# Performance work log

Measured on AMD Instinct MI355X. Metric: run time of the kernel, lower is better.

The kernel has to match this reference:

```python
import jax, jax.numpy as jnp
import numpy as np

GAMMA = 1.4
CFL = 0.5
DX = 1e-3
ENTROPY_FIX = 0.1
NX = 1048576


def _roe_flux(rL, uL, pL, rR, uR, pR):
    """Roe flux with Harten entropy fix, vectorized over all interfaces."""
    g = GAMMA
    EL = pL / (g - 1) + 0.5 * rL * uL * uL
    ER = pR / (g - 1) + 0.5 * rR * uR * uR
    HL = (EL + pL) / rL
    HR = (ER + pR) / rR
    sL = jnp.sqrt(rL)
    sR = jnp.sqrt(rR)
    den = sL + sR
    ur = (sL * uL + sR * uR) / den
    Hr = (sL * HL + sR * HR) / den
    c = jnp.sqrt(jnp.clip((g - 1) * (Hr - 0.5 * ur * ur), 1e-10))
    eps = ENTROPY_FIX * c
    l1 = ur - c
    l3 = ur + c
    a1 = jnp.sqrt(l1 * l1 + eps * eps)
    a2 = jnp.sqrt(ur * ur + eps * eps)
    a3 = jnp.sqrt(l3 * l3 + eps * eps)
    drho = rR - rL
    du = uR - uL
    dp = pR - pL
    c2 = c * c
    al2 = drho - dp / c2
    al1 = (dp - c * rR * du) / (2 * c2)
    al3 = (dp + c * rR * du) / (2 * c2)
    FrL = rL * uL; FmL = rL * uL * uL + pL; FeL = uL * (EL + pL)
    FrR = rR * uR; FmR = rR * uR * uR + pR; FeR = uR * (ER + pR)
    dr = a1 * al1 + a2 * al2 + a3 * al3
    dm = a1 * al1 * l1 + a2 * al2 * ur + a3 * al3 * l3
    de = (a1 * al1 * (Hr - ur * c) + a2 * al2 * 0.5 * ur * ur
          + a3 * al3 * (Hr + ur * c))
    return (0.5 * (FrL + FrR - dr),
            0.5 * (FmL + FmR - dm),
            0.5 * (FeL + FeR - de))


def _step(carry, t_final):
    """One first-order Euler timestep with CFL-adaptive dt clipped to t_final."""
    rho, rhou, E, t = carry
    g = GAMMA
    u = rhou / rho
    p = (g - 1) * (E - 0.5 * rho * u * u)
    c = jnp.sqrt(g * p / rho)
    dt = CFL * DX / jnp.max(jnp.abs(u) + c)
    dt = jnp.minimum(dt, jnp.maximum(t_final - t, 0.0))
    # replicate edge ghost cells: [nx] -> [nx+2]
    rp = jnp.concatenate([rho[:1], rho, rho[-1:]])
    up = jnp.concatenate([u[:1], u, u[-1:]])
    pp = jnp.concatenate([p[:1], p, p[-1:]])
    # nx+1 interface fluxes
    Fr, Fm, Fe = _roe_flux(rp[:-1], up[:-1], pp[:-1], rp[1:], up[1:], pp[1:])
    dtdx = dt / DX
    return (rho - dtdx * (Fr[1:] - Fr[:-1]),
            rhou - dtdx * (Fm[1:] - Fm[:-1]),
            E - dtdx * (Fe[1:] - Fe[:-1]),
            t + dt)


def setup_inputs() -> dict:
    key = jax.random.key(0)
    k1, k2, k3 = jax.random.split(key, 3)
    rho = 1.0 + 0.5 * jax.random.uniform(k1, (NX,), jnp.float32)
    u = 0.1 * jax.random.normal(k2, (NX,), jnp.float32)
    p = 1.0 + 0.5 * jax.random.uniform(k3, (NX,), jnp.float32)
    return {"rho_init": rho, "u_init": u, "p_init": p,
            "t_final": jnp.float32(10.0), "n_steps": 32}


def reference(rho_init, u_init, p_init, t_final, n_steps):
    g = GAMMA
    rho = rho_init
    rhou = rho_init * u_init
    E = p_init / (g - 1) + 0.5 * rho_init * u_init ** 2
    body = jax.checkpoint(lambda c, _: (_step(c, t_final), None))
    (rho, rhou, E, _), _ = jax.lax.scan(
        body, (rho, rhou, E, jnp.float32(0.0)), None, length=n_steps)
    u = rhou / rho
    p = (g - 1) * (E - 0.5 * rho * u * u)
    return rho, u, p
```

## Files before the change

kernel.cpp:

```cpp
#include <hip/hip_runtime.h>


#define NXC   1048576
#define GAM   1.4f
#define GM1   0.4f
#define IGM1  2.5f
#define CFLC  0.5f
#define DXC   1e-3f
#define IDXC  1000.0f
#define EFIX  0.1f
#define NSTEPS 32
#define NSLOT  (NSTEPS + 1)

#define ABLK  1024
#define ACPT  4
#define ATILE (ABLK*ACPT)
#define ANBLK (NXC/ATILE)

#define CTRL_TOTAL (NSLOT * ANBLK)

__device__ __forceinline__ float frcp(float x){ return __builtin_amdgcn_rcpf(x); }
__device__ __forceinline__ float frsq(float x){ return __builtin_amdgcn_rsqf(x); }
__device__ __forceinline__ float fsqrt_(float x){ return __builtin_amdgcn_sqrtf(x); }

__device__ __forceinline__ float devloadf(const float* p) {
    return __hip_atomic_load(p, __ATOMIC_RELAXED, __HIP_MEMORY_SCOPE_AGENT);
}
__device__ __forceinline__ void devstoref(float* p, float v) {
    __hip_atomic_store(p, v, __ATOMIC_RELAXED, __HIP_MEMORY_SCOPE_AGENT);
}
__device__ __forceinline__ unsigned devloadu(const unsigned* p) {
    return __hip_atomic_load(p, __ATOMIC_RELAXED, __HIP_MEMORY_SCOPE_AGENT);
}
__device__ __forceinline__ void devstoreu(unsigned* p, unsigned v) {
    __hip_atomic_store(p, v, __ATOMIC_RELAXED, __HIP_MEMORY_SCOPE_AGENT);
}

__device__ __forceinline__ float wave_max(float v) {
    #pragma unroll
    for (int k = 32; k >= 1; k >>= 1)
        v = fmaxf(v, __shfl_xor(v, k));
    return v;
}

__global__ void bmax_init(unsigned* z) {
    int i = blockIdx.x * 256 + threadIdx.x;
    if (i < CTRL_TOTAL) z[i] = 0xAAAAAAAAu;
}

__device__ __forceinline__ void roe(
        float rL, float uL, float pL, float sL, float gL,
        float rR, float uR, float pR, float sR, float gR,
        float& Frj, float& Fmj, float& Fej) {
    float invden = frcp(sL + sR);
    float ur = (sL * uL + sR * uR) * invden;
    float Hr = (gL + gR) * invden;
    float c2u = fmaxf(GM1 * (Hr - 0.5f * ur * ur), 1e-10f);
    float qc = frsq(c2u);
    float c  = c2u * qc;
    float inv2c2 = 0.5f * qc * qc;
    float eps = EFIX * c;
    float l1 = ur - c, l3 = ur + c;
    float a1 = fsqrt_(l1 * l1 + eps * eps);
    float a2 = fsqrt_(ur * ur + eps * eps);
    float a3 = fsqrt_(l3 * l3 + eps * eps);
    float drho = rR - rL;
    float du   = uR - uL;
    float dp   = pR - pL;
    float al2 = drho - (dp + dp) * inv2c2;
    float tcd = c * rR * du;
    float al1 = (dp - tcd) * inv2c2;
    float al3 = (dp + tcd) * inv2c2;
    float FrL = rL * uL, FrR = rR * uR;
    float FmL = FrL * uL + pL, FmR = FrR * uR + pR;
    float FeL = uL * (gL * sL), FeR = uR * (gR * sR);
    float w1 = a1 * al1, w2 = a2 * al2, w3 = a3 * al3;
    Frj = 0.5f * (FrL + FrR - (w1 + w2 + w3));
    Fmj = 0.5f * (FmL + FmR - (w1 * l1 + w2 * ur + w3 * l3));
    Fej = 0.5f * (FeL + FeR - (w1 * (Hr - ur * c) + w2 * (0.5f * ur * ur)
                               + w3 * (Hr + ur * c)));
}

__global__ __launch_bounds__(ABLK, 4) void euler_async(
        const float* __restrict__ rho0, const float* __restrict__ u0,
        const float* __restrict__ p0, const float* __restrict__ tf,
        float* __restrict__ out, unsigned* __restrict__ bmax,
        float* __restrict__ halo) {
    __shared__ float Lr[ABLK], Lu[ABLK], Lp[ABLK];
    __shared__ float fxr[ABLK], fxm[ABLK], fxe[ABLK];
    __shared__ float red[ABLK / 64];
    __shared__ float samax;

    const int tid = threadIdx.x;
    const int lb = (blockIdx.x & 7) * (ANBLK / 8) + (blockIdx.x >> 3);
    const int c0 = lb * ATILE + ACPT * tid;
    const int lane = tid & 63, wid = tid >> 6;

    float cr[4], cu[4], cp[4], cE[4], cs[4], cg[4];

    {
        float4 r4 = *(const float4*)(rho0 + c0);
        float4 u4 = *(const float4*)(u0 + c0);
        float4 p4 = *(const float4*)(p0 + c0);
        cr[0]=r4.x; cr[1]=r4.y; cr[2]=r4.z; cr[3]=r4.w;
        cu[0]=u4.x; cu[1]=u4.y; cu[2]=u4.z; cu[3]=u4.w;
        cp[0]=p4.x; cp[1]=p4.y; cp[2]=p4.z; cp[3]=p4.w;
        float nm = 0.f;
        #pragma unroll
        for (int c = 0; c < 4; ++c) {
            float E = cp[c] * IGM1 + 0.5f * cr[c] * cu[c] * cu[c];
            float q = frsq(cr[c]);
            cE[c] = E;
            cs[c] = cr[c] * q;
            cg[c] = (E + cp[c]) * q;
            nm = fmaxf(nm, fabsf(cu[c]) + fsqrt_(GAM * cp[c] * (q * q)));
        }
        Lr[tid]=cr[3]; Lu[tid]=cu[3]; Lp[tid]=cp[3];
        if (tid == 0) {
            float* h = halo + (size_t)lb * 6;
            devstoref(h, cr[0]); devstoref(h+1, cu[0]); devstoref(h+2, cp[0]);
        }
        if (tid == ABLK - 1) {
            float* h = halo + (size_t)lb * 6 + 3;
            devstoref(h, cr[3]); devstoref(h+1, cu[3]); devstoref(h+2, cp[3]);
        }
        nm = wave_max(nm);
        if (lane == 0) red[wid] = nm;
        __syncthreads();
        if (tid < ABLK / 64) {
            float bm = red[tid];
            bm = fmaxf(bm, __shfl_xor(bm, 8));
            bm = fmaxf(bm, __shfl_xor(bm, 4));
            bm = fmaxf(bm, __shfl_xor(bm, 2));
            bm = fmaxf(bm, __shfl_xor(bm, 1));
            if (tid == 0) devstoreu(&bmax[lb], __float_as_uint(bm));
        }
    }
    float t = 0.f;
    const float tfin = *tf;

    for (int k = 0; k < NSTEPS; ++k) {
        const unsigned* brow = bmax + (size_t)k * ANBLK;
        const unsigned* brdt = bmax + (size_t)(k > 0 ? k - 1 : 0) * ANBLK;
        float Fr[5], Fm[5], Fe[5];

        float rl, ul, pl;
        float r5 = 0.f, u5 = 0.f, p5 = 0.f;
        if (tid == 0) {
            if (lb > 0) {
                while (devloadu(&brow[lb - 1]) & 0x80000000u)
                    __builtin_amdgcn_s_sleep(1);
                const float* h = halo + ((size_t)k * ANBLK + (lb - 1)) * 6 + 3;
                rl = devloadf(h); ul = devloadf(h+1); pl = devloadf(h+2);
            } else { rl = cr[0]; ul = cu[0]; pl = cp[0]; }
        } else { rl = Lr[tid-1]; ul = Lu[tid-1]; pl = Lp[tid-1]; }
        if (tid == ABLK - 1) {
            if (lb < ANBLK - 1) {
                while (devloadu(&brow[lb + 1]) & 0x80000000u)
                    __builtin_amdgcn_s_sleep(1);
                const float* h = halo + ((size_t)k * ANBLK + (lb + 1)) * 6;
                r5 = devloadf(h); u5 = devloadf(h+1); p5 = devloadf(h+2);
            } else { r5 = cr[3]; u5 = cu[3]; p5 = cp[3]; }
        }

        roe(cr[0],cu[0],cp[0],cs[0],cg[0], cr[1],cu[1],cp[1],cs[1],cg[1],
            Fr[1], Fm[1], Fe[1]);
        roe(cr[1],cu[1],cp[1],cs[1],cg[1], cr[2],cu[2],cp[2],cs[2],cg[2],
            Fr[2], Fm[2], Fe[2]);
        roe(cr[2],cu[2],cp[2],cs[2],cg[2], cr[3],cu[3],cp[3],cs[3],cg[3],
            Fr[3], Fm[3], Fe[3]);

        {
            float El = pl * IGM1 + 0.5f * rl * ul * ul;
            float ql = frsq(rl);
            float sl = rl * ql, gl = (El + pl) * ql;
            roe(rl,ul,pl,sl,gl, cr[0],cu[0],cp[0],cs[0],cg[0],
                Fr[0], Fm[0], Fe[0]);
            fxr[tid] = Fr[0]; fxm[tid] = Fm[0]; fxe[tid] = Fe[0];
        }

        if (tid == ABLK - 1) {
            float E5 = p5 * IGM1 + 0.5f * r5 * u5 * u5;
            float q5 = frsq(r5);
            float s5 = r5 * q5, g5 = (E5 + p5) * q5;
            roe(cr[3],cu[3],cp[3],cs[3],cg[3], r5,u5,p5,s5,g5,
                Fr[4], Fm[4], Fe[4]);
        }

        if (wid == 0) {
            unsigned v0, v1, v2, v3;
            for (;;) {
                v0 = devloadu(&brdt[lane]);
                v1 = devloadu(&brdt[64 + lane]);
                v2 = devloadu(&brdt[128 + lane]);
                v3 = devloadu(&brdt[192 + lane]);
                if (__all(((v0 | v1 | v2 | v3) & 0x80000000u) == 0u)) break;
                __builtin_amdgcn_s_sleep(1);
            }
            float m = fmaxf(fmaxf(__uint_as_float(v0), __uint_as_float(v1)),
                            fmaxf(__uint_as_float(v2), __uint_as_float(v3)));
            m = wave_max(m);
            if (lane == 0) samax = m;
        }

        __syncthreads();

        if (tid < ABLK - 1) {
            Fr[4] = fxr[tid + 1]; Fm[4] = fxm[tid + 1]; Fe[4] = fxe[tid + 1];
        }
        float amax = samax;
        float dt = fminf((CFLC * DXC) * frcp(amax), fmaxf(tfin - t, 0.f));
        t += dt;
        float dtdx = dt * IDXC;

        float nm = 0.f;
        #pragma unroll
        for (int c = 0; c < 4; ++c) {
            float r2 = cr[c]         - dtdx * (Fr[c+1] - Fr[c]);
            float m2 = cr[c] * cu[c] - dtdx * (Fm[c+1] - Fm[c]);
            float E2 = cE[c]         - dtdx * (Fe[c+1] - Fe[c]);
            float q2 = frsq(r2);
            float ir = q2 * q2;
            float u2 = m2 * ir;
            float p2 = GM1 * (E2 - 0.5f * r2 * u2 * u2);
            cr[c]=r2; cu[c]=u2; cp[c]=p2; cE[c]=E2;
            cs[c]=r2 * q2;
            cg[c]=(E2 + p2) * q2;
            nm = fmaxf(nm, fabsf(u2) + fsqrt_(GAM * p2 * ir));
        }

        if (k < NSTEPS - 1) {
            Lr[tid]=cr[3]; Lu[tid]=cu[3]; Lp[tid]=cp[3];
            if (tid == 0) {
                float* h = halo + ((size_t)(k + 1) * ANBLK + lb) * 6;
                devstoref(h, cr[0]); devstoref(h+1, cu[0]); devstoref(h+2, cp[0]);
            }
            if (tid == ABLK - 1) {
                float* h = halo + ((size_t)(k + 1) * ANBLK + lb) * 6 + 3;
                devstoref(h, cr[3]); devstoref(h+1, cu[3]); devstoref(h+2, cp[3]);
            }
            nm = wave_max(nm);
            if (lane == 0) red[wid] = nm;
            __syncthreads();
            if (tid < ABLK / 64) {
                float bm = red[tid];
                bm = fmaxf(bm, __shfl_xor(bm, 8));
                bm = fmaxf(bm, __shfl_xor(bm, 4));
                bm = fmaxf(bm, __shfl_xor(bm, 2));
                bm = fmaxf(bm, __shfl_xor(bm, 1));
                if (tid == 0)
                    devstoreu(&bmax[(size_t)(k + 1) * ANBLK + lb],
                              __float_as_uint(bm));
            }
        } else {
            *(float4*)(out + c0)         = make_float4(cr[0], cr[1], cr[2], cr[3]);
            *(float4*)(out + NXC + c0)   = make_float4(cu[0], cu[1], cu[2], cu[3]);
            *(float4*)(out + 2*NXC + c0) = make_float4(cp[0], cp[1], cp[2], cp[3]);
        }
    }
}

extern "C" void kernel_launch(void* const* d_in, const int* in_sizes, int n_in,
                              void* d_out, int out_size, void* d_ws, size_t ws_size,
                              hipStream_t stream) {
    const float* rho0 = (const float*)d_in[0];
    const float* u0   = (const float*)d_in[1];
    const float* p0   = (const float*)d_in[2];
    const float* tf   = (const float*)d_in[3];

    float* out      = (float*)d_out;
    unsigned* bmax  = (unsigned*)d_ws;
    float* halo     = (float*)(bmax + CTRL_TOTAL);

    bmax_init<<<(CTRL_TOTAL + 255) / 256, 256, 0, stream>>>(bmax);

    void* args[] = {(void*)&rho0, (void*)&u0, (void*)&p0, (void*)&tf,
                    (void*)&out, (void*)&bmax, (void*)&halo};
    hipLaunchCooperativeKernel((void*)euler_async, dim3(ANBLK), dim3(ABLK),
                               args, 0, stream);
}
```

Before: 203.1 us.

## Exchange neighbor states via wave shuffles and drop one block barrier per step

Replaces the per-thread shared-memory exchange of left-neighbor states and interface fluxes with intra-wave shuffles, passing only wave-boundary values through small double-buffered shared arrays. This removes one __syncthreads per timestep, and every wave now polls the global block-max array itself, with loads issued early so they overlap the Roe flux work. The block-reduction result is written by wave 8 instead of wave 0, moving that work off wave 0, which holds the halo thread. The costs are more global polling traffic, since all 16 waves per block read 256 entries, and reliance on double buffering for correctness.

```diff
diff --git a/kernel.cpp b/kernel.cpp
--- a/kernel.cpp
+++ b/kernel.cpp
@@ -16,6 +16,7 @@
 #define ACPT  4
 #define ATILE (ABLK*ACPT)
 #define ANBLK (NXC/ATILE)
+#define NWAVE (ABLK/64)
 
 #define CTRL_TOTAL (NSLOT * ANBLK)
 
@@ -86,10 +87,9 @@
         const float* __restrict__ p0, const float* __restrict__ tf,
         float* __restrict__ out, unsigned* __restrict__ bmax,
         float* __restrict__ halo) {
-    __shared__ float Lr[ABLK], Lu[ABLK], Lp[ABLK];
-    __shared__ float fxr[ABLK], fxm[ABLK], fxe[ABLK];
-    __shared__ float red[ABLK / 64];
-    __shared__ float samax;
+    __shared__ float W3[2][NWAVE][5];
+    __shared__ float R0[2][NWAVE][5];
+    __shared__ float red[2][NWAVE];
 
     const int tid = threadIdx.x;
     const int lb = (blockIdx.x & 7) * (ANBLK / 8) + (blockIdx.x >> 3);
@@ -115,7 +115,14 @@
             cg[c] = (E + cp[c]) * q;
             nm = fmaxf(nm, fabsf(cu[c]) + fsqrt_(GAM * cp[c] * (q * q)));
         }
-        Lr[tid]=cr[3]; Lu[tid]=cu[3]; Lp[tid]=cp[3];
+        if (lane == 63) {
+            W3[0][wid][0]=cr[3]; W3[0][wid][1]=cu[3]; W3[0][wid][2]=cp[3];
+            W3[0][wid][3]=cs[3]; W3[0][wid][4]=cg[3];
+        }
+        if (lane == 0) {
+            R0[0][wid][0]=cr[0]; R0[0][wid][1]=cu[0]; R0[0][wid][2]=cp[0];
+            R0[0][wid][3]=cs[0]; R0[0][wid][4]=cg[0];
+        }
         if (tid == 0) {
             float* h = halo + (size_t)lb * 6;
             devstoref(h, cr[0]); devstoref(h+1, cu[0]); devstoref(h+2, cp[0]);
@@ -125,15 +132,15 @@
             devstoref(h, cr[3]); devstoref(h+1, cu[3]); devstoref(h+2, cp[3]);
         }
         nm = wave_max(nm);
-        if (lane == 0) red[wid] = nm;
+        if (lane == 0) red[0][wid] = nm;
         __syncthreads();
-        if (tid < ABLK / 64) {
-            float bm = red[tid];
+        if (wid == 8 && lane < NWAVE) {
+            float bm = red[0][lane];
             bm = fmaxf(bm, __shfl_xor(bm, 8));
             bm = fmaxf(bm, __shfl_xor(bm, 4));
             bm = fmaxf(bm, __shfl_xor(bm, 2));
             bm = fmaxf(bm, __shfl_xor(bm, 1));
-            if (tid == 0) devstoreu(&bmax[lb], __float_as_uint(bm));
+            if (lane == 0) devstoreu(&bmax[lb], __float_as_uint(bm));
         }
     }
     float t = 0.f;
@@ -142,26 +149,59 @@
     for (int k = 0; k < NSTEPS; ++k) {
         const unsigned* brow = bmax + (size_t)k * ANBLK;
         const unsigned* brdt = bmax + (size_t)(k > 0 ? k - 1 : 0) * ANBLK;
+        const int kb = k & 1;
         float Fr[5], Fm[5], Fe[5];
 
-        float rl, ul, pl;
-        float r5 = 0.f, u5 = 0.f, p5 = 0.f;
-        if (tid == 0) {
-            if (lb > 0) {
-                while (devloadu(&brow[lb - 1]) & 0x80000000u)
-                    __builtin_amdgcn_s_sleep(1);
-                const float* h = halo + ((size_t)k * ANBLK + (lb - 1)) * 6 + 3;
-                rl = devloadf(h); ul = devloadf(h+1); pl = devloadf(h+2);
-            } else { rl = cr[0]; ul = cu[0]; pl = cp[0]; }
-        } else { rl = Lr[tid-1]; ul = Lu[tid-1]; pl = Lp[tid-1]; }
-        if (tid == ABLK - 1) {
-            if (lb < ANBLK - 1) {
-                while (devloadu(&brow[lb + 1]) & 0x80000000u)
-                    __builtin_amdgcn_s_sleep(1);
-                const float* h = halo + ((size_t)k * ANBLK + (lb + 1)) * 6;
-                r5 = devloadf(h); u5 = devloadf(h+1); p5 = devloadf(h+2);
-            } else { r5 = cr[3]; u5 = cu[3]; p5 = cp[3]; }
-        }
+        unsigned pv0 = devloadu(&brdt[lane]);
+        unsigned pv1 = devloadu(&brdt[64 + lane]);
+        unsigned pv2 = devloadu(&brdt[128 + lane]);
+        unsigned pv3 = devloadu(&brdt[192 + lane]);
+
+        float wl0, wl1, wl2, wl3, wl4;
+        if (lane == 0) {
+            if (tid == 0) {
+                if (lb > 0) {
+                    while (devloadu(&brow[lb - 1]) & 0x80000000u)
+                        __builtin_amdgcn_s_sleep(1);
+                    const float* h = halo + ((size_t)k * ANBLK + (lb - 1)) * 6 + 3;
+                    wl0 = devloadf(h); wl1 = devloadf(h+1); wl2 = devloadf(h+2);
+                    float El = wl2 * IGM1 + 0.5f * wl0 * wl1 * wl1;
+                    float ql = frsq(wl0);
+                    wl3 = wl0 * ql; wl4 = (El + wl2) * ql;
+                } else {
+                    wl0 = cr[0]; wl1 = cu[0]; wl2 = cp[0];
+                    wl3 = cs[0]; wl4 = cg[0];
+                }
+            } else {
+                const float* w = W3[kb][wid - 1];
+                wl0 = w[0]; wl1 = w[1]; wl2 = w[2]; wl3 = w[3]; wl4 = w[4];
+            }
+        }
+        float wr0, wr1, wr2, wr3, wr4;
+        if (lane == 63) {
+            if (tid == ABLK - 1) {
+                if (lb < ANBLK - 1) {
+                    while (devloadu(&brow[lb + 1]) & 0x80000000u)
+                        __builtin_amdgcn_s_sleep(1);
+                    const float* h = halo + ((size_t)k * ANBLK + (lb + 1)) * 6;
+                    wr0 = devloadf(h); wr1 = devloadf(h+1); wr2 = devloadf(h+2);
+                    float E5 = wr2 * IGM1 + 0.5f * wr0 * wr1 * wr1;
+                    float q5 = frsq(wr0);
+                    wr3 = wr0 * q5; wr4 = (E5 + wr2) * q5;
+                } else {
+                    wr0 = cr[3]; wr1 = cu[3]; wr2 = cp[3];
+                    wr3 = cs[3]; wr4 = cg[3];
+                }
+            } else {
+                const float* w = R0[kb][wid + 1];
+                wr0 = w[0]; wr1 = w[1]; wr2 = w[2]; wr3 = w[3]; wr4 = w[4];
+            }
+        }
+
+        float rl = __shfl_up(cr[3], 1), ul = __shfl_up(cu[3], 1);
+        float pl = __shfl_up(cp[3], 1);
+        float sl = __shfl_up(cs[3], 1), gl = __shfl_up(cg[3], 1);
+        if (lane == 0) { rl = wl0; ul = wl1; pl = wl2; sl = wl3; gl = wl4; }
 
         roe(cr[0],cu[0],cp[0],cs[0],cg[0], cr[1],cu[1],cp[1],cs[1],cg[1],
             Fr[1], Fm[1], Fe[1]);
@@ -169,47 +209,28 @@
             Fr[2], Fm[2], Fe[2]);
         roe(cr[2],cu[2],cp[2],cs[2],cg[2], cr[3],cu[3],cp[3],cs[3],cg[3],
             Fr[3], Fm[3], Fe[3]);
-
-        {
-            float El = pl * IGM1 + 0.5f * rl * ul * ul;
-            float ql = frsq(rl);
-            float sl = rl * ql, gl = (El + pl) * ql;
-            roe(rl,ul,pl,sl,gl, cr[0],cu[0],cp[0],cs[0],cg[0],
-                Fr[0], Fm[0], Fe[0]);
-            fxr[tid] = Fr[0]; fxm[tid] = Fm[0]; fxe[tid] = Fe[0];
-        }
-
-        if (tid == ABLK - 1) {
-            float E5 = p5 * IGM1 + 0.5f * r5 * u5 * u5;
-            float q5 = frsq(r5);
-            float s5 = r5 * q5, g5 = (E5 + p5) * q5;
-            roe(cr[3],cu[3],cp[3],cs[3],cg[3], r5,u5,p5,s5,g5,
+        roe(rl,ul,pl,sl,gl, cr[0],cu[0],cp[0],cs[0],cg[0],
+            Fr[0], Fm[0], Fe[0]);
+
+        Fr[4] = __shfl_down(Fr[0], 1);
+        Fm[4] = __shfl_down(Fm[0], 1);
+        Fe[4] = __shfl_down(Fe[0], 1);
+        if (lane == 63) {
+            roe(cr[3],cu[3],cp[3],cs[3],cg[3], wr0,wr1,wr2,wr3,wr4,
                 Fr[4], Fm[4], Fe[4]);
         }
 
-        if (wid == 0) {
-            unsigned v0, v1, v2, v3;
-            for (;;) {
-                v0 = devloadu(&brdt[lane]);
-                v1 = devloadu(&brdt[64 + lane]);
-                v2 = devloadu(&brdt[128 + lane]);
-                v3 = devloadu(&brdt[192 + lane]);
-                if (__all(((v0 | v1 | v2 | v3) & 0x80000000u) == 0u)) break;
-                __builtin_amdgcn_s_sleep(1);
-            }
-            float m = fmaxf(fmaxf(__uint_as_float(v0), __uint_as_float(v1)),
-                            fmaxf(__uint_as_float(v2), __uint_as_float(v3)));
-            m = wave_max(m);
-            if (lane == 0) samax = m;
-        }
-
-        __syncthreads();
-
-        if (tid < ABLK - 1) {
-            Fr[4] = fxr[tid + 1]; Fm[4] = fxm[tid + 1]; Fe[4] = fxe[tid + 1];
-        }
-        float amax = samax;
-        float dt = fminf((CFLC * DXC) * frcp(amax), fmaxf(tfin - t, 0.f));
+        while (!__all(((pv0 | pv1 | pv2 | pv3) & 0x80000000u) == 0u)) {
+            __builtin_amdgcn_s_sleep(1);
+            pv0 = devloadu(&brdt[lane]);
+            pv1 = devloadu(&brdt[64 + lane]);
+            pv2 = devloadu(&brdt[128 + lane]);
+            pv3 = devloadu(&brdt[192 + lane]);
+        }
+        float m = fmaxf(fmaxf(__uint_as_float(pv0), __uint_as_float(pv1)),
+                        fmaxf(__uint_as_float(pv2), __uint_as_float(pv3)));
+        m = wave_max(m);
+        float dt = fminf((CFLC * DXC) * frcp(m), fmaxf(tfin - t, 0.f));
         t += dt;
         float dtdx = dt * IDXC;
 
@@ -230,7 +251,15 @@
         }
 
         if (k < NSTEPS - 1) {
-            Lr[tid]=cr[3]; Lu[tid]=cu[3]; Lp[tid]=cp[3];
+            const int nb = (k + 1) & 1;
+            if (lane == 63) {
+                W3[nb][wid][0]=cr[3]; W3[nb][wid][1]=cu[3]; W3[nb][wid][2]=cp[3];
+                W3[nb][wid][3]=cs[3]; W3[nb][wid][4]=cg[3];
+            }
+            if (lane == 0) {
+                R0[nb][wid][0]=cr[0]; R0[nb][wid][1]=cu[0]; R0[nb][wid][2]=cp[0];
+                R0[nb][wid][3]=cs[0]; R0[nb][wid][4]=cg[0];
+            }
             if (tid == 0) {
                 float* h = halo + ((size_t)(k + 1) * ANBLK + lb) * 6;
                 devstoref(h, cr[0]); devstoref(h+1, cu[0]); devstoref(h+2, cp[0]);
@@ -240,15 +269,15 @@
                 devstoref(h, cr[3]); devstoref(h+1, cu[3]); devstoref(h+2, cp[3]);
             }
             nm = wave_max(nm);
-            if (lane == 0) red[wid] = nm;
+            if (lane == 0) red[nb][wid] = nm;
             __syncthreads();
-            if (tid < ABLK / 64) {
-                float bm = red[tid];
+            if (wid == 8 && lane < NWAVE) {
+                float bm = red[nb][lane];
                 bm = fmaxf(bm, __shfl_xor(bm, 8));
                 bm = fmaxf(bm, __shfl_xor(bm, 4));
                 bm = fmaxf(bm, __shfl_xor(bm, 2));
                 bm = fmaxf(bm, __shfl_xor(bm, 1));
-                if (tid == 0)
+                if (lane == 0)
                     devstoreu(&bmax[(size_t)(k + 1) * ANBLK + lb],
                               __float_as_uint(bm));
             }
```

After: 331.2 us. +63.1%, slower.
